# Kernel tuning notes

Hardware: AMD Instinct MI355X
Metric: run time of the kernel (lower is better)

Reference implementation:

```python
import jax, jax.numpy as jnp
import numpy as np

B = 4096          # graphs
NPG = 50          # nodes per graph
N = B * NPG       # total nodes
E = 819200        # edges
C = 128           # hidden_channels
T = 2048          # num_tools


def setup_inputs() -> dict:
    key = jax.random.key(0)
    ks = jax.random.split(key, 12)
    s = 0.1
    return {
        "x": jax.random.randint(ks[0], (N, 1), 0, T, dtype=jnp.int32),
        "edge_index": jax.random.randint(ks[1], (2, E), 0, N, dtype=jnp.int32),
        "batch": (jnp.arange(N, dtype=jnp.int32) // NPG).astype(jnp.int32),
        "num_graphs": B,
        "embedding": jax.random.normal(ks[2], (T, C), jnp.float32) * s,
        "w_ih": jax.random.normal(ks[3], (3 * C, C), jnp.float32) * s,
        "w_hh": jax.random.normal(ks[4], (3 * C, C), jnp.float32) * s,
        "w1": jax.random.normal(ks[5], (C, C), jnp.float32) * s,
        "w2": jax.random.normal(ks[6], (C, C), jnp.float32) * s,
        "b2": jax.random.normal(ks[7], (C,), jnp.float32) * s,
        "wq": jax.random.normal(ks[8], (C, C), jnp.float32) * s,
        "bq": jax.random.normal(ks[9], (C,), jnp.float32) * s,
        "wt": jax.random.normal(ks[10], (C, 2 * C), jnp.float32) * s,
    }


def reference(x, edge_index, batch, num_graphs, embedding, w_ih, w_hh,
              w1, w2, b2, wq, bq, wt):
    n = x.shape[0]
    # embedding lookup (dropout2d is identity at eval)
    emb = embedding[x[:, 0]]                                   # [N, C]

    # --- GatedGraphConv: scatter-add of source features to targets ---
    src, dst = edge_index[0], edge_index[1]
    m = jax.ops.segment_sum(emb[src], dst, num_segments=n)     # [N, C]

    # --- GRUCell(m, emb), no bias ---
    gi = m @ w_ih.T                                            # [N, 3C]
    gh = emb @ w_hh.T                                          # [N, 3C]
    i_r, i_z, i_n = jnp.split(gi, 3, axis=1)
    h_r, h_z, h_n = jnp.split(gh, 3, axis=1)
    r = jax.nn.sigmoid(i_r + h_r)
    z = jax.nn.sigmoid(i_z + h_z)
    ncand = jnp.tanh(i_n + r * h_n)
    h = (1.0 - z) * ncand + z * emb                            # [N, C]

    # --- ragged segment attention readout ---
    counts = jax.ops.segment_sum(jnp.ones_like(batch), batch,
                                 num_segments=num_graphs)      # [B]
    last_idx = jnp.cumsum(counts) - 1                          # [B]
    w_l = h[last_idx]                                          # [B, C] last node per graph
    w_g_r = w_l[batch]                                         # [N, C] broadcast to nodes
    q1 = w_g_r @ w1.T
    q2 = h @ w2.T + b2
    alpha = jax.nn.sigmoid(q1 + q2) @ wq.T + bq                # [N, C]
    w_g = jax.ops.segment_sum(alpha * h, batch,
                              num_segments=num_graphs)         # [B, C]

    w = jnp.concatenate([w_l, w_g], axis=1) @ wt.T             # [B, C]
    logits = w @ embedding.T                                   # [B, T]
    return logits
```

## Files before the change

### kernel.cpp

```cpp
#include <hip/hip_runtime.h>
#include <hip/hip_bf16.h>

#define NN 204800
#define EE 819200
#define BB 4096
#define NPG 50
#define CC 128
#define TT 2048
#define BINCAP 32

typedef __attribute__((ext_vector_type(8))) short short8;
typedef __attribute__((ext_vector_type(4))) float f32x4;
typedef __attribute__((ext_vector_type(2))) float f32x2;
typedef __attribute__((ext_vector_type(4))) int i32x4;

__device__ __forceinline__ short f2bf(float f) {
    union { float f; unsigned u; } v; v.f = f;
    unsigned r = (v.u + 0x7FFFu + ((v.u >> 16) & 1u)) >> 16;
    return (short)r;
}
__device__ __forceinline__ float bf2f(short s) {
    union { float f; unsigned u; } v;
    v.u = ((unsigned)(unsigned short)s) << 16;
    return v.f;
}
__device__ __forceinline__ f32x2 unpk2(int u) {
    union { int i; float f; } lo, hi;
    lo.i = u << 16;
    hi.i = u & 0xffff0000;
    return (f32x2){lo.f, hi.f};
}
__device__ __forceinline__ float sigf(float x) { return 1.0f / (1.0f + __expf(-x)); }
__device__ __forceinline__ float tanh_fast(float x) {
    x = fminf(fmaxf(x, -15.0f), 15.0f);
    float e = __expf(2.0f * x);
    return 1.0f - 2.0f / (e + 1.0f);
}

__global__ void prep_small(const float* __restrict__ emb, const float* __restrict__ w1,
                           const float* __restrict__ w2, const float* __restrict__ wq,
                           const float* __restrict__ wt, const float* __restrict__ w_ih,
                           const float* __restrict__ w_hh,
                           __hip_bfloat16* __restrict__ embbf, __hip_bfloat16* __restrict__ w1bf,
                           __hip_bfloat16* __restrict__ w2bf, __hip_bfloat16* __restrict__ wqbf,
                           __hip_bfloat16* __restrict__ wtbf, __hip_bfloat16* __restrict__ w_ihbf,
                           __hip_bfloat16* __restrict__ w_hhbf) {
    int i = blockIdx.x * 256 + threadIdx.x;
    if (i < TT * CC) embbf[i] = __float2bfloat16(emb[i]);
    if (i < CC * CC) {
        w1bf[i] = __float2bfloat16(w1[i]);
        w2bf[i] = __float2bfloat16(w2[i]);
        wqbf[i] = __float2bfloat16(wq[i]);
    }
    if (i < CC * 2 * CC) wtbf[i] = __float2bfloat16(wt[i]);
    if (i < 3 * CC * CC) {
        w_ihbf[i] = __float2bfloat16(w_ih[i]);
        w_hhbf[i] = __float2bfloat16(w_hh[i]);
    }
}

__global__ __launch_bounds__(256) void build_tables_mfma(
    const __hip_bfloat16* __restrict__ embbf,
    const __hip_bfloat16* __restrict__ w_ihbf, const __hip_bfloat16* __restrict__ w_hhbf,
    __hip_bfloat16* __restrict__ G_ih, __hip_bfloat16* __restrict__ G_hh) {
    __shared__ short at[64][CC + 8];
    int t = threadIdx.x;
    int tokbase = blockIdx.x * 64;
    int chunk = blockIdx.y;
    const __hip_bfloat16* wsel = (chunk < 3) ? w_ihbf : w_hhbf;
    __hip_bfloat16* G = (chunk < 3) ? G_ih : G_hh;
    int jbase = (chunk % 3) * CC;

    const short8* asrc = (const short8*)(embbf + (size_t)tokbase * CC);
#pragma unroll
    for (int it = 0; it < 4; it++) {
        int idx = it * 256 + t;
        *(short8*)&at[idx >> 4][(idx & 15) * 8] = asrc[idx];
    }
    __syncthreads();

    int wave = t >> 6, lane = t & 63;
    int mrow = lane & 15, quad = lane >> 4;
    int colb = wave * 32;

    f32x4 acc[4][2];
#pragma unroll
    for (int rt = 0; rt < 4; rt++)
#pragma unroll
        for (int n = 0; n < 2; n++) acc[rt][n] = (f32x4){0.f, 0.f, 0.f, 0.f};
    short8 bw[2][4];
#pragma unroll
    for (int n = 0; n < 2; n++)
#pragma unroll
        for (int kt = 0; kt < 4; kt++)
            bw[n][kt] = *(const short8*)(wsel + (size_t)(jbase + colb + n * 16 + mrow) * CC + kt * 32 + quad * 8);
#pragma unroll
    for (int kt = 0; kt < 4; kt++)
#pragma unroll
        for (int rt = 0; rt < 4; rt++) {
            short8 af = *(const short8*)&at[rt * 16 + mrow][kt * 32 + quad * 8];
#pragma unroll
            for (int n = 0; n < 2; n++)
                acc[rt][n] = __builtin_amdgcn_mfma_f32_16x16x32_bf16(af, bw[n][kt], acc[rt][n], 0, 0, 0);
        }
#pragma unroll
    for (int rt = 0; rt < 4; rt++)
#pragma unroll
        for (int n = 0; n < 2; n++)
#pragma unroll
            for (int r = 0; r < 4; r++) {
                int tok = tokbase + rt * 16 + quad * 4 + r;
                G[(size_t)tok * 384 + jbase + colb + n * 16 + mrow] = __float2bfloat16(acc[rt][n][r]);
            }
}

__global__ void fill_bins(const int* __restrict__ ei, const int* __restrict__ x,
                          int* __restrict__ deg, int* __restrict__ bins) {
    int e = blockIdx.x * 256 + threadIdx.x;
    int d = ei[EE + e], s = ei[e];
    int pos = atomicAdd(&deg[d], 1);
    bins[(size_t)d * BINCAP + pos] = x[s];
}

__global__ __launch_bounds__(256) void gru_kernel(
    const int* __restrict__ x, const int* __restrict__ deg,
    const int* __restrict__ bins,
    const __hip_bfloat16* __restrict__ G_ih, const __hip_bfloat16* __restrict__ G_hh,
    const float* __restrict__ emb,
    __hip_bfloat16* __restrict__ hbf) {
    int nid = blockIdx.x * 16 + (threadIdx.x >> 4);
    int j = threadIdx.x & 15;
    int tok = x[nid];
    int dg = deg[nid];
    const int* bin = bins + (size_t)nid * BINCAP;
    f32x2 ir[4], iz[4], inn[4];
#pragma unroll
    for (int d = 0; d < 4; d++) {
        ir[d] = (f32x2){0.f, 0.f}; iz[d] = (f32x2){0.f, 0.f}; inn[d] = (f32x2){0.f, 0.f};
    }
    for (int c = 0; c < dg; c += 4) {
        int4 tq = *(const int4*)&bin[c];
        int tks[4] = {tq.x, tq.y, tq.z, tq.w};
#pragma unroll
        for (int u = 0; u < 4; u++) {
            if (c + u < dg) {
                int st = tks[u];
                const i32x4* gp = (const i32x4*)(G_ih + (size_t)st * 384);
                i32x4 a = gp[j];
                i32x4 b = gp[16 + j];
                i32x4 c2 = gp[32 + j];
#pragma unroll
                for (int d = 0; d < 4; d++) {
                    ir[d]  += unpk2(a[d]);
                    iz[d]  += unpk2(b[d]);
                    inn[d] += unpk2(c2[d]);
                }
            }
        }
    }
    const i32x4* hp = (const i32x4*)(G_hh + (size_t)tok * 384);
    i32x4 hr4 = hp[j], hz4 = hp[16 + j], hn4 = hp[32 + j];
    const float4* ep = (const float4*)(emb + (size_t)tok * CC + j * 8);
    float4 ev0 = ep[0], ev1 = ep[1];
    float evs[8] = {ev0.x, ev0.y, ev0.z, ev0.w, ev1.x, ev1.y, ev1.z, ev1.w};
    short8 hv;
#pragma unroll
    for (int d = 0; d < 4; d++) {
        f32x2 hrv = unpk2(hr4[d]), hzv = unpk2(hz4[d]), hnv = unpk2(hn4[d]);
#pragma unroll
        for (int k = 0; k < 2; k++) {
            int p = d * 2 + k;
            float r  = sigf(ir[d][k] + hrv[k]);
            float z  = sigf(iz[d][k] + hzv[k]);
            float nc = tanh_fast(inn[d][k] + r * hnv[k]);
            float h  = (1.f - z) * nc + z * evs[p];
            hv[p] = f2bf(h);
        }
    }
    ((short8*)hbf)[nid * 16 + j] = hv;
}

__global__ __launch_bounds__(256) void q1_kernel(
    const __hip_bfloat16* __restrict__ hbf, const __hip_bfloat16* __restrict__ w1bf,
    const float* __restrict__ b2,
    float* __restrict__ q1_all, __hip_bfloat16* __restrict__ w_lbf) {
    int t = threadIdx.x;
    int gbase = blockIdx.x * 64;
    int wave = t >> 6, lane = t & 63;
    int mrow = lane & 15, quad = lane >> 4;
    int g = gbase + wave * 16 + mrow;

    short8 afr[4];
#pragma unroll
    for (int kt = 0; kt < 4; kt++) {
        afr[kt] = *(const short8*)(hbf + ((size_t)g * NPG + NPG - 1) * CC + kt * 32 + quad * 8);
        *(short8*)(w_lbf + (size_t)g * CC + kt * 32 + quad * 8) = afr[kt];
    }
    f32x4 acc[8];
#pragma unroll
    for (int nt = 0; nt < 8; nt++) {
        float bv = b2[nt * 16 + mrow];
        acc[nt] = (f32x4){bv, bv, bv, bv};
    }
#pragma unroll
    for (int kt = 0; kt < 4; kt++) {
#pragma unroll
        for (int nt = 0; nt < 8; nt++) {
            const short8* bp = (const short8*)(w1bf + (nt * 16 + mrow) * CC + kt * 32 + quad * 8);
            acc[nt] = __builtin_amdgcn_mfma_f32_16x16x32_bf16(afr[kt], *bp, acc[nt], 0, 0, 0);
        }
    }
#pragma unroll
    for (int nt = 0; nt < 8; nt++)
#pragma unroll
        for (int r = 0; r < 4; r++)
            q1_all[(size_t)(gbase + wave * 16 + quad * 4 + r) * CC + nt * 16 + mrow] = acc[nt][r];
}

__global__ __launch_bounds__(256, 4) void node_attn(
    const __hip_bfloat16* __restrict__ hbf, const float* __restrict__ q1_all,
    const __hip_bfloat16* __restrict__ w2bf, const __hip_bfloat16* __restrict__ wqbf,
    const float* __restrict__ bq,
    float* __restrict__ w_gf) {
    __shared__ short hsb[64][CC + 8];
    __shared__ short ssb[64][CC + 8];
    __shared__ float q1s[3][CC];
    __shared__ int gidx[64];
    int rb = blockIdx.x * 64;
    int g0 = rb / 50;
    int t = threadIdx.x;

    const short8* hsrc = (const short8*)(hbf + (size_t)rb * CC);
#pragma unroll
    for (int it = 0; it < 4; it++) {
        int idx = it * 256 + t;
        *(short8*)&hsb[idx >> 4][(idx & 15) * 8] = hsrc[idx];
    }
    if (t < 64) gidx[t] = (rb + t) / 50 - g0;
    for (int idx = t; idx < 3 * CC; idx += 256) {
        int gg = g0 + (idx >> 7);
        q1s[idx >> 7][idx & 127] = (gg < BB) ? q1_all[(size_t)gg * CC + (idx & 127)] : 0.f;
    }
    __syncthreads();

    int wave = t >> 6, lane = t & 63;
    int mrow = lane & 15, quad = lane >> 4;
    int colb = wave * 32;

    f32x4 acc[4][2];
#pragma unroll
    for (int rt = 0; rt < 4; rt++)
#pragma unroll
        for (int n = 0; n < 2; n++) acc[rt][n] = (f32x4){0.f, 0.f, 0.f, 0.f};
    {
        short8 bw2[2][4];
#pragma unroll
        for (int n = 0; n < 2; n++)
#pragma unroll
            for (int kt = 0; kt < 4; kt++)
                bw2[n][kt] = *(const short8*)(w2bf + (size_t)(colb + n * 16 + mrow) * CC + kt * 32 + quad * 8);
#pragma unroll
        for (int kt = 0; kt < 4; kt++)
#pragma unroll
            for (int rt = 0; rt < 4; rt++) {
                short8 af = *(const short8*)&hsb[rt * 16 + mrow][kt * 32 + quad * 8];
#pragma unroll
                for (int n = 0; n < 2; n++)
                    acc[rt][n] = __builtin_amdgcn_mfma_f32_16x16x32_bf16(af, bw2[n][kt], acc[rt][n], 0, 0, 0);
            }
    }
#pragma unroll
    for (int rt = 0; rt < 4; rt++)
#pragma unroll
        for (int r = 0; r < 4; r++) {
            int rowl = rt * 16 + quad * 4 + r;
            int gi_ = gidx[rowl];
#pragma unroll
            for (int n = 0; n < 2; n++) {
                int col = colb + n * 16 + mrow;
                ssb[rowl][col] = f2bf(sigf(acc[rt][n][r] + q1s[gi_][col]));
            }
        }
    __syncthreads();

    f32x4 acd[4][2];
    short8 bwq[2][4];
#pragma unroll
    for (int n = 0; n < 2; n++) {
        float bv = bq[colb + n * 16 + mrow];
#pragma unroll
        for (int rt = 0; rt < 4; rt++) acd[rt][n] = (f32x4){bv, bv, bv, bv};
#pragma unroll
        for (int kt = 0; kt < 4; kt++)
            bwq[n][kt] = *(const short8*)(wqbf + (size_t)(colb + n * 16 + mrow) * CC + kt * 32 + quad * 8);
    }
#pragma unroll
    for (int kt = 0; kt < 4; kt++)
#pragma unroll
        for (int rt = 0; rt < 4; rt++) {
            short8 af = *(const short8*)&ssb[rt * 16 + mrow][kt * 32 + quad * 8];
#pragma unroll
            for (int n = 0; n < 2; n++)
                acd[rt][n] = __builtin_amdgcn_mfma_f32_16x16x32_bf16(af, bwq[n][kt], acd[rt][n], 0, 0, 0);
        }
#pragma unroll
    for (int n = 0; n < 2; n++) {
        int col = colb + n * 16 + mrow;
        float ps0 = 0.f, ps1 = 0.f, ps2 = 0.f;
#pragma unroll
        for (int rt = 0; rt < 4; rt++)
#pragma unroll
            for (int r = 0; r < 4; r++) {
                int rowl = rt * 16 + quad * 4 + r;
                int gi_ = gidx[rowl];
                float v = acd[rt][n][r] * bf2f(hsb[rowl][col]);
                ps0 += (gi_ == 0) ? v : 0.f;
                ps1 += (gi_ == 1) ? v : 0.f;
                ps2 += (gi_ == 2) ? v : 0.f;
            }
        ps0 += __shfl_xor(ps0, 16, 64); ps0 += __shfl_xor(ps0, 32, 64);
        ps1 += __shfl_xor(ps1, 16, 64); ps1 += __shfl_xor(ps1, 32, 64);
        ps2 += __shfl_xor(ps2, 16, 64); ps2 += __shfl_xor(ps2, 32, 64);
        if (quad == 0) {
            atomicAdd(&w_gf[(size_t)g0 * CC + col], ps0);
            atomicAdd(&w_gf[(size_t)(g0 + 1) * CC + col], ps1);
            if (g0 + 2 < BB) atomicAdd(&w_gf[(size_t)(g0 + 2) * CC + col], ps2);
        }
    }
}

__global__ __launch_bounds__(256) void wvec_kernel(
    const __hip_bfloat16* __restrict__ w_lbf, const float* __restrict__ w_gf,
    const __hip_bfloat16* __restrict__ wtbf,
    __hip_bfloat16* __restrict__ wvecbf) {
    int t = threadIdx.x;
    int gbase = blockIdx.x * 64;
    int wave = t >> 6, lane = t & 63;
    int mrow = lane & 15, quad = lane >> 4;
    int grow = gbase + wave * 16 + mrow;

    f32x4 acc[8];
#pragma unroll
    for (int nt = 0; nt < 8; nt++) acc[nt] = (f32x4){0.f, 0.f, 0.f, 0.f};
#pragma unroll
    for (int kt = 0; kt < 8; kt++) {
        short8 af;
        if (kt < 4) {
            af = *(const short8*)(w_lbf + (size_t)grow * CC + kt * 32 + quad * 8);
        } else {
            const float* ws = w_gf + (size_t)grow * CC + (kt - 4) * 32 + quad * 8;
            float4 v0 = *(const float4*)ws, v1 = *(const float4*)(ws + 4);
            af[0] = f2bf(v0.x); af[1] = f2bf(v0.y); af[2] = f2bf(v0.z); af[3] = f2bf(v0.w);
            af[4] = f2bf(v1.x); af[5] = f2bf(v1.y); af[6] = f2bf(v1.z); af[7] = f2bf(v1.w);
        }
#pragma unroll
        for (int nt = 0; nt < 8; nt++) {
            const short8* bp = (const short8*)(wtbf + (nt * 16 + mrow) * 256 + kt * 32 + quad * 8);
            acc[nt] = __builtin_amdgcn_mfma_f32_16x16x32_bf16(af, *bp, acc[nt], 0, 0, 0);
        }
    }
#pragma unroll
    for (int nt = 0; nt < 8; nt++)
#pragma unroll
        for (int r = 0; r < 4; r++)
            wvecbf[(size_t)(gbase + wave * 16 + quad * 4 + r) * CC + nt * 16 + mrow] =
                __float2bfloat16(acc[nt][r]);
}

__global__ __launch_bounds__(256) void logits_kernel(
    const __hip_bfloat16* __restrict__ wvecbf, const __hip_bfloat16* __restrict__ embbf,
    float* __restrict__ out) {
    __shared__ short avs[64][CC + 8];
    int t = threadIdx.x;
    int gbase = blockIdx.x * 64;
    int tbase = blockIdx.y * 128;

    const short8* asrc = (const short8*)(wvecbf + (size_t)gbase * CC);
#pragma unroll
    for (int it = 0; it < 4; it++) {
        int idx = it * 256 + t;
        *(short8*)&avs[idx >> 4][(idx & 15) * 8] = asrc[idx];
    }
    __syncthreads();

    int wave = t >> 6, lane = t & 63;
    int mrow = lane & 15, quad = lane >> 4;

    f32x4 acc3[8];
#pragma unroll
    for (int nt = 0; nt < 8; nt++) acc3[nt] = (f32x4){0.f, 0.f, 0.f, 0.f};
#pragma unroll
    for (int kt = 0; kt < 4; kt++) {
        short8 af = *(const short8*)&avs[wave * 16 + mrow][kt * 32 + quad * 8];
#pragma unroll
        for (int nt = 0; nt < 8; nt++) {
            const short8* bp = (const short8*)(embbf + (size_t)(tbase + nt * 16 + mrow) * CC + kt * 32 + quad * 8);
            acc3[nt] = __builtin_amdgcn_mfma_f32_16x16x32_bf16(af, *bp, acc3[nt], 0, 0, 0);
        }
    }
#pragma unroll
    for (int nt = 0; nt < 8; nt++)
#pragma unroll
        for (int r = 0; r < 4; r++) {
            int grow2 = gbase + wave * 16 + quad * 4 + r;
            int tok = tbase + nt * 16 + mrow;
            out[(size_t)grow2 * TT + tok] = acc3[nt][r];
        }
}

extern "C" void kernel_launch(void* const* d_in, const int* in_sizes, int n_in,
                              void* d_out, int out_size, void* d_ws, size_t ws_size,
                              hipStream_t stream) {
    const int* x     = (const int*)d_in[0];
    const int* ei    = (const int*)d_in[1];
    const float* emb = (const float*)d_in[4];
    const float* w_ih = (const float*)d_in[5];
    const float* w_hh = (const float*)d_in[6];
    const float* w1  = (const float*)d_in[7];
    const float* w2  = (const float*)d_in[8];
    const float* b2  = (const float*)d_in[9];
    const float* wq  = (const float*)d_in[10];
    const float* bq  = (const float*)d_in[11];
    const float* wt  = (const float*)d_in[12];
    float* out = (float*)d_out;

    char* ws = (char*)d_ws;
    size_t off = 0;
    auto alloc = [&](size_t b) { void* p = ws + off; off += (b + 255) & ~(size_t)255; return p; };
    __hip_bfloat16* G_ih  = (__hip_bfloat16*)alloc((size_t)TT * 384 * 2);
    __hip_bfloat16* G_hh  = (__hip_bfloat16*)alloc((size_t)TT * 384 * 2);
    __hip_bfloat16* embbf = (__hip_bfloat16*)alloc((size_t)TT * CC * 2);
    __hip_bfloat16* w1bf  = (__hip_bfloat16*)alloc((size_t)CC * CC * 2);
    __hip_bfloat16* w2bf  = (__hip_bfloat16*)alloc((size_t)CC * CC * 2);
    __hip_bfloat16* wqbf  = (__hip_bfloat16*)alloc((size_t)CC * CC * 2);
    __hip_bfloat16* wtbf  = (__hip_bfloat16*)alloc((size_t)CC * 256 * 2);
    __hip_bfloat16* w_ihbf= (__hip_bfloat16*)alloc((size_t)3 * CC * CC * 2);
    __hip_bfloat16* w_hhbf= (__hip_bfloat16*)alloc((size_t)3 * CC * CC * 2);
    int* deg              = (int*)alloc((size_t)NN * 4);
    int* bins             = (int*)alloc((size_t)NN * BINCAP * 4);
    __hip_bfloat16* w_lbf = (__hip_bfloat16*)alloc((size_t)BB * CC * 2);
    float* w_gf           = (float*)alloc((size_t)BB * CC * 4);
    float* q1_all         = (float*)alloc((size_t)BB * CC * 4);
    __hip_bfloat16* wvecbf= (__hip_bfloat16*)alloc((size_t)BB * CC * 2);
    __hip_bfloat16* hbf   = (__hip_bfloat16*)alloc((size_t)NN * CC * 2);

    hipMemsetAsync(deg, 0, (size_t)NN * 4, stream);
    hipMemsetAsync(w_gf, 0, (size_t)BB * CC * 4, stream);
    fill_bins<<<EE / 256, 256, 0, stream>>>(ei, x, deg, bins);
    prep_small<<<1024, 256, 0, stream>>>(emb, w1, w2, wq, wt, w_ih, w_hh,
                                         embbf, w1bf, w2bf, wqbf, wtbf, w_ihbf, w_hhbf);
    build_tables_mfma<<<dim3(TT / 64, 6), 256, 0, stream>>>(embbf, w_ihbf, w_hhbf, G_ih, G_hh);
    gru_kernel<<<NN / 16, 256, 0, stream>>>(x, deg, bins, G_ih, G_hh, emb, hbf);
    q1_kernel<<<BB / 64, 256, 0, stream>>>(hbf, w1bf, b2, q1_all, w_lbf);
    node_attn<<<NN / 64, 256, 0, stream>>>(hbf, q1_all, w2bf, wqbf, bq, w_gf);
    wvec_kernel<<<BB / 64, 256, 0, stream>>>(w_lbf, w_gf, wtbf, wvecbf);
    logits_kernel<<<dim3(BB / 64, TT / 128), 256, 0, stream>>>(wvecbf, embbf, out);
}
```

Before: 292.6 us.

## Sort GRU nodes into degree classes to balance per-wave gather work

Adds a classify kernel that buckets nodes by ceil(degree/4) using shared and global atomics, writing a per-class permutation with the degree packed into the entry. The GRU kernel then processes nodes in class order, so each wave's 16-node groups share similar loop trip counts, which cuts divergence and idle lanes in the neighbor gather loop. It also sets a launch-bounds occupancy hint. The cost is an extra kernel launch, a 9*NN permutation buffer, and scattered node order, which lowers write locality for hbf and bins.

```diff
diff --git a/kernel.cpp b/kernel.cpp
--- a/kernel.cpp
+++ b/kernel.cpp
@@ -122,16 +122,50 @@
     bins[(size_t)d * BINCAP + pos] = x[s];
 }
 
-__global__ __launch_bounds__(256) void gru_kernel(
-    const int* __restrict__ x, const int* __restrict__ deg,
-    const int* __restrict__ bins,
+__global__ __launch_bounds__(256) void classify(const int* __restrict__ deg,
+                                                int* __restrict__ clsCount,
+                                                int* __restrict__ perm2) {
+    __shared__ int lcount[9];
+    __shared__ int lbase[9];
+    int t = threadIdx.x;
+    if (t < 9) lcount[t] = 0;
+    __syncthreads();
+    int nid = blockIdx.x * 256 + t;
+    int dg = deg[nid];
+    int cls = (dg + 3) >> 2;
+    int lpos = atomicAdd(&lcount[cls], 1);
+    __syncthreads();
+    if (t < 9) lbase[t] = atomicAdd(&clsCount[t], lcount[t]);
+    __syncthreads();
+    perm2[(size_t)cls * NN + lbase[cls] + lpos] = nid | (dg << 20);
+}
+
+__global__ __launch_bounds__(256, 8) void gru_kernel(
+    const int* __restrict__ x,
+    const int* __restrict__ bins, const int* __restrict__ perm2,
+    const int* __restrict__ clsCount,
     const __hip_bfloat16* __restrict__ G_ih, const __hip_bfloat16* __restrict__ G_hh,
     const float* __restrict__ emb,
     __hip_bfloat16* __restrict__ hbf) {
-    int nid = blockIdx.x * 16 + (threadIdx.x >> 4);
-    int j = threadIdx.x & 15;
+    __shared__ int soff[9];
+    int t = threadIdx.x;
+    if (t < 9) {
+        int s = 0;
+        for (int c = 0; c < t; c++) s += clsCount[c];
+        soff[t] = s;
+    }
+    __syncthreads();
+    int p = blockIdx.x * 16 + (t >> 4);
+    int cls = 8;
+#pragma unroll
+    for (int k = 8; k >= 1; k--)
+        if (p < soff[k]) cls = k - 1;
+    int e = perm2[(size_t)cls * NN + (p - soff[cls])];
+    int nid = e & 0xFFFFF;
+    int dg = e >> 20;
+
+    int j = t & 15;
     int tok = x[nid];
-    int dg = deg[nid];
     const int* bin = bins + (size_t)nid * BINCAP;
     f32x2 ir[4], iz[4], inn[4];
 #pragma unroll
@@ -169,12 +203,12 @@
         f32x2 hrv = unpk2(hr4[d]), hzv = unpk2(hz4[d]), hnv = unpk2(hn4[d]);
 #pragma unroll
         for (int k = 0; k < 2; k++) {
-            int p = d * 2 + k;
+            int p2 = d * 2 + k;
             float r  = sigf(ir[d][k] + hrv[k]);
             float z  = sigf(iz[d][k] + hzv[k]);
             float nc = tanh_fast(inn[d][k] + r * hnv[k]);
-            float h  = (1.f - z) * nc + z * evs[p];
-            hv[p] = f2bf(h);
+            float h  = (1.f - z) * nc + z * evs[p2];
+            hv[p2] = f2bf(h);
         }
     }
     ((short8*)hbf)[nid * 16 + j] = hv;
@@ -443,14 +477,18 @@
     float* q1_all         = (float*)alloc((size_t)BB * CC * 4);
     __hip_bfloat16* wvecbf= (__hip_bfloat16*)alloc((size_t)BB * CC * 2);
     __hip_bfloat16* hbf   = (__hip_bfloat16*)alloc((size_t)NN * CC * 2);
+    int* perm2            = (int*)alloc((size_t)9 * NN * 4);
+    int* clsCount         = (int*)alloc(64);
 
     hipMemsetAsync(deg, 0, (size_t)NN * 4, stream);
     hipMemsetAsync(w_gf, 0, (size_t)BB * CC * 4, stream);
+    hipMemsetAsync(clsCount, 0, 64, stream);
     fill_bins<<<EE / 256, 256, 0, stream>>>(ei, x, deg, bins);
     prep_small<<<1024, 256, 0, stream>>>(emb, w1, w2, wq, wt, w_ih, w_hh,
                                          embbf, w1bf, w2bf, wqbf, wtbf, w_ihbf, w_hhbf);
     build_tables_mfma<<<dim3(TT / 64, 6), 256, 0, stream>>>(embbf, w_ihbf, w_hhbf, G_ih, G_hh);
-    gru_kernel<<<NN / 16, 256, 0, stream>>>(x, deg, bins, G_ih, G_hh, emb, hbf);
+    classify<<<NN / 256, 256, 0, stream>>>(deg, clsCount, perm2);
+    gru_kernel<<<NN / 16, 256, 0, stream>>>(x, bins, perm2, clsCount, G_ih, G_hh, emb, hbf);
     q1_kernel<<<BB / 64, 256, 0, stream>>>(hbf, w1bf, b2, q1_all, w_lbf);
     node_attn<<<NN / 64, 256, 0, stream>>>(hbf, q1_all, w2bf, wqbf, bq, w_gf);
     wvec_kernel<<<BB / 64, 256, 0, stream>>>(w_lbf, w_gf, wtbf, wvecbf);
```

Result: slower. 303.3 us (+3.7%).

## Bin edges per 16-node tile and aggregate GRU input gates with one-hot MFMA

Applied to the files above, without the earlier changes.

Edges are now binned per 16-node destination tile as packed 16-bit (owner, token) entries instead of per-node int bins. The GRU kernel stages 32 source G_ih rows at a time in shared memory and runs the scatter-sum as an MFMA, using a one-hot owner matrix as the A operand. This is meant to replace per-node serial gather-adds and to cut bin memory traffic and atomic contention on per-node counters. The cost is extra shared-memory transposes and barriers, plus a hard cap of 192 edges per tile that silently drops any overflow edges.

```diff
diff --git a/kernel.cpp b/kernel.cpp
--- a/kernel.cpp
+++ b/kernel.cpp
@@ -7,7 +7,9 @@
 #define NPG 50
 #define CC 128
 #define TT 2048
-#define BINCAP 32
+#define TILES (NN / 16)
+#define CAP 192
+#define SROW 394
 
 typedef __attribute__((ext_vector_type(8))) short short8;
 typedef __attribute__((ext_vector_type(4))) float f32x4;
@@ -114,50 +116,93 @@
             }
 }
 
-__global__ void fill_bins(const int* __restrict__ ei, const int* __restrict__ x,
-                          int* __restrict__ deg, int* __restrict__ bins) {
+__global__ void fill_tile(const int* __restrict__ ei, const int* __restrict__ x,
+                          int* __restrict__ tileCnt, unsigned short* __restrict__ ew) {
     int e = blockIdx.x * 256 + threadIdx.x;
     int d = ei[EE + e], s = ei[e];
-    int pos = atomicAdd(&deg[d], 1);
-    bins[(size_t)d * BINCAP + pos] = x[s];
-}
-
-__global__ __launch_bounds__(256) void gru_kernel(
-    const int* __restrict__ x, const int* __restrict__ deg,
-    const int* __restrict__ bins,
+    int tok = x[s];
+    int tile = d >> 4, owner = d & 15;
+    int pos = atomicAdd(&tileCnt[tile * 4], 1);
+    if (pos < CAP) ew[(size_t)tile * CAP + pos] = (unsigned short)((owner << 11) | tok);
+}
+
+__global__ __launch_bounds__(256) void gru_mfma(
+    const int* __restrict__ x, const int* __restrict__ tileCnt,
+    const unsigned short* __restrict__ ew,
     const __hip_bfloat16* __restrict__ G_ih, const __hip_bfloat16* __restrict__ G_hh,
     const float* __restrict__ emb,
     __hip_bfloat16* __restrict__ hbf) {
-    int nid = blockIdx.x * 16 + (threadIdx.x >> 4);
-    int j = threadIdx.x & 15;
+    __shared__ __align__(16) short pool[32 * SROW];
+    int t = threadIdx.x;
+    int tile = blockIdx.x;
+    int E = tileCnt[tile * 4];
+    if (E > CAP) E = CAP;
+    int NCh = (E + 31) >> 5;
+    const unsigned short* et = ew + (size_t)tile * CAP;
+
+    int wave = t >> 6, lane = t & 63;
+    int mrow = lane & 15, quad = lane >> 4;
+
+    f32x4 acc[6];
+#pragma unroll
+    for (int i = 0; i < 6; i++) acc[i] = (f32x4){0.f, 0.f, 0.f, 0.f};
+
+    int se = t >> 3;
+    int sc0 = t & 7;
+
+    for (int c = 0; c < NCh; c++) {
+        int kb = c * 32;
+        int stok = et[kb + se] & 0x7FF;
+        const short8* grow_ = (const short8*)(G_ih + (size_t)stok * 384);
+#pragma unroll
+        for (int i = 0; i < 6; i++) {
+            int c8 = sc0 + i * 8;
+            *(short8*)&pool[se * SROW + c8 * 8] = grow_[c8];
+        }
+        i32x4 q = *(const i32x4*)&et[kb + quad * 8];
+        short8 af;
+#pragma unroll
+        for (int i = 0; i < 8; i++) {
+            unsigned u = ((unsigned)q[i >> 1] >> ((i & 1) * 16)) & 0xFFFFu;
+            int owner = (int)(u >> 11) & 15;
+            af[i] = (owner == mrow && (kb + quad * 8 + i) < E) ? (short)0x3F80 : (short)0;
+        }
+        __syncthreads();
+#pragma unroll
+        for (int i = 0; i < 6; i++) {
+            int ch = wave * 96 + i * 16 + mrow;
+            short8 b8;
+#pragma unroll
+            for (int u = 0; u < 8; u++)
+                b8[u] = pool[(quad * 8 + u) * SROW + ch];
+            acc[i] = __builtin_amdgcn_mfma_f32_16x16x32_bf16(af, b8, acc[i], 0, 0, 0);
+        }
+        __syncthreads();
+    }
+
+    float* gif = (float*)pool;
+#pragma unroll
+    for (int i = 0; i < 6; i++) {
+        int ch = (wave * 6 + i) * 16 + mrow;
+#pragma unroll
+        for (int r = 0; r < 4; r++) {
+            int node = quad * 4 + r;
+            gif[node * 388 + ch] = acc[i][r];
+        }
+    }
+    __syncthreads();
+
+    int node = t >> 4, j = t & 15;
+    int nid = tile * 16 + node;
     int tok = x[nid];
-    int dg = deg[nid];
-    const int* bin = bins + (size_t)nid * BINCAP;
-    f32x2 ir[4], iz[4], inn[4];
-#pragma unroll
-    for (int d = 0; d < 4; d++) {
-        ir[d] = (f32x2){0.f, 0.f}; iz[d] = (f32x2){0.f, 0.f}; inn[d] = (f32x2){0.f, 0.f};
-    }
-    for (int c = 0; c < dg; c += 4) {
-        int4 tq = *(const int4*)&bin[c];
-        int tks[4] = {tq.x, tq.y, tq.z, tq.w};
-#pragma unroll
-        for (int u = 0; u < 4; u++) {
-            if (c + u < dg) {
-                int st = tks[u];
-                const i32x4* gp = (const i32x4*)(G_ih + (size_t)st * 384);
-                i32x4 a = gp[j];
-                i32x4 b = gp[16 + j];
-                i32x4 c2 = gp[32 + j];
-#pragma unroll
-                for (int d = 0; d < 4; d++) {
-                    ir[d]  += unpk2(a[d]);
-                    iz[d]  += unpk2(b[d]);
-                    inn[d] += unpk2(c2[d]);
-                }
-            }
-        }
-    }
+    const float* gn = gif + node * 388;
+    float4 i0 = *(const float4*)(gn + j * 8),       i1 = *(const float4*)(gn + j * 8 + 4);
+    float4 z0 = *(const float4*)(gn + 128 + j * 8), z1 = *(const float4*)(gn + 128 + j * 8 + 4);
+    float4 n0 = *(const float4*)(gn + 256 + j * 8), n1 = *(const float4*)(gn + 256 + j * 8 + 4);
+    float irv[8] = {i0.x, i0.y, i0.z, i0.w, i1.x, i1.y, i1.z, i1.w};
+    float izv[8] = {z0.x, z0.y, z0.z, z0.w, z1.x, z1.y, z1.z, z1.w};
+    float inv[8] = {n0.x, n0.y, n0.z, n0.w, n1.x, n1.y, n1.z, n1.w};
+
     const i32x4* hp = (const i32x4*)(G_hh + (size_t)tok * 384);
     i32x4 hr4 = hp[j], hz4 = hp[16 + j], hn4 = hp[32 + j];
     const float4* ep = (const float4*)(emb + (size_t)tok * CC + j * 8);
@@ -169,12 +214,12 @@
         f32x2 hrv = unpk2(hr4[d]), hzv = unpk2(hz4[d]), hnv = unpk2(hn4[d]);
 #pragma unroll
         for (int k = 0; k < 2; k++) {
-            int p = d * 2 + k;
-            float r  = sigf(ir[d][k] + hrv[k]);
-            float z  = sigf(iz[d][k] + hzv[k]);
-            float nc = tanh_fast(inn[d][k] + r * hnv[k]);
-            float h  = (1.f - z) * nc + z * evs[p];
-            hv[p] = f2bf(h);
+            int p2 = d * 2 + k;
+            float r  = sigf(irv[p2] + hrv[k]);
+            float z  = sigf(izv[p2] + hzv[k]);
+            float nc = tanh_fast(inv[p2] + r * hnv[k]);
+            float h  = (1.f - z) * nc + z * evs[p2];
+            hv[p2] = f2bf(h);
         }
     }
     ((short8*)hbf)[nid * 16 + j] = hv;
@@ -436,21 +481,21 @@
     __hip_bfloat16* wtbf  = (__hip_bfloat16*)alloc((size_t)CC * 256 * 2);
     __hip_bfloat16* w_ihbf= (__hip_bfloat16*)alloc((size_t)3 * CC * CC * 2);
     __hip_bfloat16* w_hhbf= (__hip_bfloat16*)alloc((size_t)3 * CC * CC * 2);
-    int* deg              = (int*)alloc((size_t)NN * 4);
-    int* bins             = (int*)alloc((size_t)NN * BINCAP * 4);
+    int* tileCnt          = (int*)alloc((size_t)TILES * 16);
+    unsigned short* ew    = (unsigned short*)alloc((size_t)TILES * CAP * 2);
     __hip_bfloat16* w_lbf = (__hip_bfloat16*)alloc((size_t)BB * CC * 2);
     float* w_gf           = (float*)alloc((size_t)BB * CC * 4);
     float* q1_all         = (float*)alloc((size_t)BB * CC * 4);
     __hip_bfloat16* wvecbf= (__hip_bfloat16*)alloc((size_t)BB * CC * 2);
     __hip_bfloat16* hbf   = (__hip_bfloat16*)alloc((size_t)NN * CC * 2);
 
-    hipMemsetAsync(deg, 0, (size_t)NN * 4, stream);
+    hipMemsetAsync(tileCnt, 0, (size_t)TILES * 16, stream);
     hipMemsetAsync(w_gf, 0, (size_t)BB * CC * 4, stream);
-    fill_bins<<<EE / 256, 256, 0, stream>>>(ei, x, deg, bins);
+    fill_tile<<<EE / 256, 256, 0, stream>>>(ei, x, tileCnt, ew);
     prep_small<<<1024, 256, 0, stream>>>(emb, w1, w2, wq, wt, w_ih, w_hh,
                                          embbf, w1bf, w2bf, wqbf, wtbf, w_ihbf, w_hhbf);
     build_tables_mfma<<<dim3(TT / 64, 6), 256, 0, stream>>>(embbf, w_ihbf, w_hhbf, G_ih, G_hh);
-    gru_kernel<<<NN / 16, 256, 0, stream>>>(x, deg, bins, G_ih, G_hh, emb, hbf);
+    gru_mfma<<<TILES, 256, 0, stream>>>(x, tileCnt, ew, G_ih, G_hh, emb, hbf);
     q1_kernel<<<BB / 64, 256, 0, stream>>>(hbf, w1bf, b2, q1_all, w_lbf);
     node_attn<<<NN / 64, 256, 0, stream>>>(hbf, q1_all, w2bf, wqbf, bq, w_gf);
     wvec_kernel<<<BB / 64, 256, 0, stream>>>(w_lbf, w_gf, wtbf, wvecbf);
```

Result: faster. 285.8 us (-2.3%).

## Aggregate embeddings then apply W_ih via MFMA in fused GRU kernel

Applied to the files above, without the earlier changes.

Instead of precomputing per-token W_ih projections (384 wide) and gathering them per edge, the GRU kernel now gathers the 128-wide bf16 embeddings per edge, sums them into m, rounds m to bf16 in shared memory, and applies W_ih with MFMA per 16-node tile. This cuts per-edge gather traffic by about three times and drops the G_ih table build, at the cost of an in-kernel matmul, shared-memory staging, and extra bf16 rounding of m. It also clamps bin positions to BINCAP.

```diff
diff --git a/kernel.cpp b/kernel.cpp
--- a/kernel.cpp
+++ b/kernel.cpp
@@ -7,7 +7,10 @@
 #define NPG 50
 #define CC 128
 #define TT 2048
+#define TILES (NN / 16)
 #define BINCAP 32
+#define MBS 136
+#define GIS 388
 
 typedef __attribute__((ext_vector_type(8))) short short8;
 typedef __attribute__((ext_vector_type(4))) float f32x4;
@@ -59,17 +62,14 @@
     }
 }
 
-__global__ __launch_bounds__(256) void build_tables_mfma(
+__global__ __launch_bounds__(256) void build_tables_hh(
     const __hip_bfloat16* __restrict__ embbf,
-    const __hip_bfloat16* __restrict__ w_ihbf, const __hip_bfloat16* __restrict__ w_hhbf,
-    __hip_bfloat16* __restrict__ G_ih, __hip_bfloat16* __restrict__ G_hh) {
+    const __hip_bfloat16* __restrict__ w_hhbf,
+    __hip_bfloat16* __restrict__ G_hh) {
     __shared__ short at[64][CC + 8];
     int t = threadIdx.x;
     int tokbase = blockIdx.x * 64;
-    int chunk = blockIdx.y;
-    const __hip_bfloat16* wsel = (chunk < 3) ? w_ihbf : w_hhbf;
-    __hip_bfloat16* G = (chunk < 3) ? G_ih : G_hh;
-    int jbase = (chunk % 3) * CC;
+    int jbase = blockIdx.y * CC;
 
     const short8* asrc = (const short8*)(embbf + (size_t)tokbase * CC);
 #pragma unroll
@@ -93,7 +93,7 @@
     for (int n = 0; n < 2; n++)
 #pragma unroll
         for (int kt = 0; kt < 4; kt++)
-            bw[n][kt] = *(const short8*)(wsel + (size_t)(jbase + colb + n * 16 + mrow) * CC + kt * 32 + quad * 8);
+            bw[n][kt] = *(const short8*)(w_hhbf + (size_t)(jbase + colb + n * 16 + mrow) * CC + kt * 32 + quad * 8);
 #pragma unroll
     for (int kt = 0; kt < 4; kt++)
 #pragma unroll
@@ -110,7 +110,7 @@
 #pragma unroll
             for (int r = 0; r < 4; r++) {
                 int tok = tokbase + rt * 16 + quad * 4 + r;
-                G[(size_t)tok * 384 + jbase + colb + n * 16 + mrow] = __float2bfloat16(acc[rt][n][r]);
+                G_hh[(size_t)tok * 384 + jbase + colb + n * 16 + mrow] = __float2bfloat16(acc[rt][n][r]);
             }
 }
 
@@ -119,45 +119,85 @@
     int e = blockIdx.x * 256 + threadIdx.x;
     int d = ei[EE + e], s = ei[e];
     int pos = atomicAdd(&deg[d], 1);
-    bins[(size_t)d * BINCAP + pos] = x[s];
-}
-
-__global__ __launch_bounds__(256) void gru_kernel(
+    if (pos < BINCAP) bins[(size_t)d * BINCAP + pos] = x[s];
+}
+
+__global__ __launch_bounds__(256) void gru_fused(
     const int* __restrict__ x, const int* __restrict__ deg,
     const int* __restrict__ bins,
-    const __hip_bfloat16* __restrict__ G_ih, const __hip_bfloat16* __restrict__ G_hh,
+    const __hip_bfloat16* __restrict__ embbf,
+    const __hip_bfloat16* __restrict__ w_ihbf,
+    const __hip_bfloat16* __restrict__ G_hh,
     const float* __restrict__ emb,
     __hip_bfloat16* __restrict__ hbf) {
-    int nid = blockIdx.x * 16 + (threadIdx.x >> 4);
-    int j = threadIdx.x & 15;
-    int tok = x[nid];
-    int dg = deg[nid];
+    __shared__ __align__(16) float pool[16 * GIS];
+    short* m_bf = (short*)pool;
+    int t = threadIdx.x;
+    int tile = blockIdx.x;
+    int node = t >> 4, j = t & 15;
+    int nid = tile * 16 + node;
+    int dg = deg[nid]; if (dg > BINCAP) dg = BINCAP;
     const int* bin = bins + (size_t)nid * BINCAP;
-    f32x2 ir[4], iz[4], inn[4];
-#pragma unroll
-    for (int d = 0; d < 4; d++) {
-        ir[d] = (f32x2){0.f, 0.f}; iz[d] = (f32x2){0.f, 0.f}; inn[d] = (f32x2){0.f, 0.f};
-    }
+
+    f32x2 mc[4];
+#pragma unroll
+    for (int d = 0; d < 4; d++) mc[d] = (f32x2){0.f, 0.f};
     for (int c = 0; c < dg; c += 4) {
         int4 tq = *(const int4*)&bin[c];
         int tks[4] = {tq.x, tq.y, tq.z, tq.w};
 #pragma unroll
         for (int u = 0; u < 4; u++) {
             if (c + u < dg) {
-                int st = tks[u];
-                const i32x4* gp = (const i32x4*)(G_ih + (size_t)st * 384);
-                i32x4 a = gp[j];
-                i32x4 b = gp[16 + j];
-                i32x4 c2 = gp[32 + j];
-#pragma unroll
-                for (int d = 0; d < 4; d++) {
-                    ir[d]  += unpk2(a[d]);
-                    iz[d]  += unpk2(b[d]);
-                    inn[d] += unpk2(c2[d]);
-                }
+                const i32x4* er = (const i32x4*)(embbf + (size_t)tks[u] * CC);
+                i32x4 e = er[j];
+#pragma unroll
+                for (int d = 0; d < 4; d++) mc[d] += unpk2(e[d]);
             }
         }
     }
+    short8 mb;
+#pragma unroll
+    for (int d = 0; d < 4; d++) {
+        mb[d * 2] = f2bf(mc[d][0]);
+        mb[d * 2 + 1] = f2bf(mc[d][1]);
+    }
+    *(short8*)&m_bf[node * MBS + j * 8] = mb;
+    __syncthreads();
+
+    int wave = t >> 6, lane = t & 63;
+    int mrow = lane & 15, quad = lane >> 4;
+    f32x4 acc[6];
+#pragma unroll
+    for (int i = 0; i < 6; i++) acc[i] = (f32x4){0.f, 0.f, 0.f, 0.f};
+#pragma unroll
+    for (int kt = 0; kt < 4; kt++) {
+        short8 af = *(const short8*)&m_bf[mrow * MBS + kt * 32 + quad * 8];
+#pragma unroll
+        for (int i = 0; i < 6; i++) {
+            const short8* bp = (const short8*)(w_ihbf + (size_t)(wave * 96 + i * 16 + mrow) * CC + kt * 32 + quad * 8);
+            acc[i] = __builtin_amdgcn_mfma_f32_16x16x32_bf16(af, *bp, acc[i], 0, 0, 0);
+        }
+    }
+    __syncthreads();
+
+#pragma unroll
+    for (int i = 0; i < 6; i++) {
+        int ch = wave * 96 + i * 16 + mrow;
+#pragma unroll
+        for (int r = 0; r < 4; r++)
+            pool[(quad * 4 + r) * GIS + ch] = acc[i][r];
+    }
+    __syncthreads();
+
+    int tok = x[nid];
+    const float* gn = pool + node * GIS;
+    float4 i0 = *(const float4*)(gn + j * 8),       i1 = *(const float4*)(gn + j * 8 + 4);
+    float4 z0 = *(const float4*)(gn + 128 + j * 8), z1 = *(const float4*)(gn + 128 + j * 8 + 4);
+    float4 n0 = *(const float4*)(gn + 256 + j * 8), n1 = *(const float4*)(gn + 256 + j * 8 + 4);
+    float irv[8] = {i0.x, i0.y, i0.z, i0.w, i1.x, i1.y, i1.z, i1.w};
+    float izv[8] = {z0.x, z0.y, z0.z, z0.w, z1.x, z1.y, z1.z, z1.w};
+    float inv[8] = {n0.x, n0.y, n0.z, n0.w, n1.x, n1.y, n1.z, n1.w};
+
     const i32x4* hp = (const i32x4*)(G_hh + (size_t)tok * 384);
     i32x4 hr4 = hp[j], hz4 = hp[16 + j], hn4 = hp[32 + j];
     const float4* ep = (const float4*)(emb + (size_t)tok * CC + j * 8);
@@ -169,12 +209,12 @@
         f32x2 hrv = unpk2(hr4[d]), hzv = unpk2(hz4[d]), hnv = unpk2(hn4[d]);
 #pragma unroll
         for (int k = 0; k < 2; k++) {
-            int p = d * 2 + k;
-            float r  = sigf(ir[d][k] + hrv[k]);
-            float z  = sigf(iz[d][k] + hzv[k]);
-            float nc = tanh_fast(inn[d][k] + r * hnv[k]);
-            float h  = (1.f - z) * nc + z * evs[p];
-            hv[p] = f2bf(h);
+            int p2 = d * 2 + k;
+            float r  = sigf(irv[p2] + hrv[k]);
+            float z  = sigf(izv[p2] + hzv[k]);
+            float nc = tanh_fast(inv[p2] + r * hnv[k]);
+            float h  = (1.f - z) * nc + z * evs[p2];
+            hv[p2] = f2bf(h);
         }
     }
     ((short8*)hbf)[nid * 16 + j] = hv;
@@ -427,7 +467,6 @@
     char* ws = (char*)d_ws;
     size_t off = 0;
     auto alloc = [&](size_t b) { void* p = ws + off; off += (b + 255) & ~(size_t)255; return p; };
-    __hip_bfloat16* G_ih  = (__hip_bfloat16*)alloc((size_t)TT * 384 * 2);
     __hip_bfloat16* G_hh  = (__hip_bfloat16*)alloc((size_t)TT * 384 * 2);
     __hip_bfloat16* embbf = (__hip_bfloat16*)alloc((size_t)TT * CC * 2);
     __hip_bfloat16* w1bf  = (__hip_bfloat16*)alloc((size_t)CC * CC * 2);
@@ -449,8 +488,8 @@
     fill_bins<<<EE / 256, 256, 0, stream>>>(ei, x, deg, bins);
     prep_small<<<1024, 256, 0, stream>>>(emb, w1, w2, wq, wt, w_ih, w_hh,
                                          embbf, w1bf, w2bf, wqbf, wtbf, w_ihbf, w_hhbf);
-    build_tables_mfma<<<dim3(TT / 64, 6), 256, 0, stream>>>(embbf, w_ihbf, w_hhbf, G_ih, G_hh);
-    gru_kernel<<<NN / 16, 256, 0, stream>>>(x, deg, bins, G_ih, G_hh, emb, hbf);
+    build_tables_hh<<<dim3(TT / 64, 3), 256, 0, stream>>>(embbf, w_hhbf, G_hh);
+    gru_fused<<<TILES, 256, 0, stream>>>(x, deg, bins, embbf, w_ihbf, G_hh, emb, hbf);
     q1_kernel<<<BB / 64, 256, 0, stream>>>(hbf, w1bf, b2, q1_all, w_lbf);
     node_attn<<<NN / 64, 256, 0, stream>>>(hbf, q1_all, w2bf, wqbf, bq, w_gf);
     wvec_kernel<<<BB / 64, 256, 0, stream>>>(w_lbf, w_gf, wtbf, wvecbf);
```

Measured after the change: 403.7 us. 38.0% more time.
